# Kernel optimization log

Measured on AMD Instinct MI355X. Metric: run time of the kernel, lower is better.

The kernel has to match this reference:

```python
import jax, jax.numpy as jnp
import numpy as np

# FP8 E4M3 spike bits [S, E3..E0, M2 M1 M0] -> exact FP32 bits [S, E7..E0, M22..M0].
# FP8 bias 7, FP32 bias 127 => normal biased-FP32 exponent = e_fp8 + 120.
# Subnormal FP8 (e==0, m>0) is normalized: leading one at mantissa bit 2/1/0 maps to
# biased exponents 120/119/118 (the circuit's e_sub constants). The 4x4 mantissa
# product (<=225) always fits exactly in the 24-bit FP32 significand, so no rounding.

def _decode(X):
    # X: [..., 8] 0/1 floats. Returns sign, 4-bit significand (8..15, leading 1 at bit3),
    # biased FP32 exponent, and nonzero flag. All float32 except the bool flag.
    s = X[..., 0]
    e = X[..., 1] * 8.0 + X[..., 2] * 4.0 + X[..., 3] * 2.0 + X[..., 4]
    m = X[..., 5] * 4.0 + X[..., 6] * 2.0 + X[..., 7]
    normal = e > 0.0
    lead2 = m >= 4.0
    lead1 = (m >= 2.0) & (m < 4.0)
    frac_sub = jnp.where(lead2, m * 2.0, jnp.where(lead1, m * 4.0, m * 8.0))
    exp_sub = jnp.where(lead2, 120.0, jnp.where(lead1, 119.0, 118.0))
    frac = jnp.where(normal, m + 8.0, frac_sub)
    exp = jnp.where(normal, e + 120.0, exp_sub)
    nonzero = normal | (m > 0.0)
    return s, frac, exp, nonzero


def _fp8_mul_to_fp32_bits(A, B):
    A, B = jnp.broadcast_arrays(A, B)
    sa, fa, ea, nza = _decode(A)
    sb, fb, eb, nzb = _decode(B)
    s_out = jnp.mod(sa + sb, 2.0)                       # XOR of sign bits
    p = fa * fb                                         # 8-bit product in [64, 225]
    e_sum = ea + eb - 127.0
    carry = p >= 128.0                                  # leading one at bit 7 vs bit 6
    exp_out = jnp.where(carry, e_sum + 1.0, e_sum)
    # align fractional bits into the 23-bit FP32 mantissa (7 or 6 fraction bits)
    mant_out = jnp.where(carry, (p - 128.0) * 65536.0, (p - 64.0) * 131072.0)
    nz = nza & nzb
    exp_out = jnp.where(nz, exp_out, 0.0)               # true zero -> exp=0, mant=0
    mant_out = jnp.where(nz, mant_out, 0.0)
    exp_pow = 2.0 ** jnp.arange(7, -1, -1, dtype=jnp.float32)
    mant_pow = 2.0 ** jnp.arange(22, -1, -1, dtype=jnp.float32)
    exp_bits = jnp.mod(jnp.floor(exp_out[..., None] / exp_pow), 2.0)
    mant_bits = jnp.mod(jnp.floor(mant_out[..., None] / mant_pow), 2.0)
    return jnp.concatenate([s_out[..., None], exp_bits, mant_bits], axis=-1)


def setup_inputs() -> dict:
    key = jax.random.key(0)
    kA, kB = jax.random.split(key)
    A = jax.random.randint(kA, (1024, 4096, 8), 0, 2).astype(jnp.float32)
    B = jax.random.randint(kB, (1024, 4096, 8), 0, 2).astype(jnp.float32)
    return {"A": A, "B": B}


def reference(A, B):
    return _fp8_mul_to_fp32_bits(A, B)
```

## Files before the change

kernel.cpp:

```cpp
#include <hip/hip_runtime.h>
#include <stdint.h>


__device__ __forceinline__ uint32_t bit_of(float f) {
    return (__float_as_uint(f) >> 23) & 1u;
}

__device__ __forceinline__ void decode8(const float4 v0, const float4 v1,
                                        uint32_t& s, int& frac, int& exp, int& nz) {
    s = bit_of(v0.x);
    int e = (int)((bit_of(v0.y) << 3) | (bit_of(v0.z) << 2) |
                  (bit_of(v0.w) << 1) |  bit_of(v1.x));
    int m = (int)((bit_of(v1.y) << 2) | (bit_of(v1.z) << 1) | bit_of(v1.w));
    int frac_sub = (m >= 4) ? (m << 1) : ((m >= 2) ? (m << 2) : (m << 3));
    int exp_sub  = (m >= 4) ? 120      : ((m >= 2) ? 119      : 118);
    bool normal = (e > 0);
    frac = normal ? (m | 8)    : frac_sub;
    exp  = normal ? (e + 120)  : exp_sub;
    nz   = ((e | m) != 0) ? 1 : 0;
}

__global__ __launch_bounds__(256) void spike_fp8_mul_kernel(
        const float4* __restrict__ A, const float4* __restrict__ B,
        float4* __restrict__ out, int n_out4) {
    int j = blockIdx.x * blockDim.x + threadIdx.x;
    if (j >= n_out4) return;
    int elem = j >> 3;
    int g    = j & 7;

    float4 a0 = A[2 * elem], a1 = A[2 * elem + 1];
    float4 b0 = B[2 * elem], b1 = B[2 * elem + 1];

    uint32_t sa, sb; int fa, ea, fb, eb, nza, nzb;
    decode8(a0, a1, sa, fa, ea, nza);
    decode8(b0, b1, sb, fb, eb, nzb);

    uint32_t sign = sa ^ sb;
    int p = fa * fb;
    int carry = p >> 7;
    int exp_out = ea + eb - 127 + carry;
    uint32_t mant = ((uint32_t)p << (17 - carry)) & 0x7fffffu;
    uint32_t bits = (sign << 31) | ((uint32_t)exp_out << 23) | mant;
    if (!(nza & nzb)) bits = sign << 31;

    int sh = 31 - (g << 2);
    float4 o;
    o.x = ((bits >> sh)       & 1u) ? 1.0f : 0.0f;
    o.y = ((bits >> (sh - 1)) & 1u) ? 1.0f : 0.0f;
    o.z = ((bits >> (sh - 2)) & 1u) ? 1.0f : 0.0f;
    o.w = ((bits >> (sh - 3)) & 1u) ? 1.0f : 0.0f;
    out[j] = o;
}

extern "C" void kernel_launch(void* const* d_in, const int* in_sizes, int n_in,
                              void* d_out, int out_size, void* d_ws, size_t ws_size,
                              hipStream_t stream) {
    const float4* A = (const float4*)d_in[0];
    const float4* B = (const float4*)d_in[1];
    float4* out     = (float4*)d_out;
    int n_out4 = out_size / 4;
    const int block = 256;
    int grid = (n_out4 + block - 1) / block;
    hipLaunchKernelGGL(spike_fp8_mul_kernel, dim3(grid), dim3(block), 0, stream,
                       A, B, out, n_out4);
}
```

Measured before the change: 694.8 us.

## Compute one element per thread and redistribute output bits via wave shuffles

Each thread now loads and decodes a single FP8 pair once instead of eight threads redundantly loading and decoding the same element. The 32 output bits are spread across the wavefront with __shfl so each store instruction writes contiguous float4s across lanes, keeping writes coalesced. This removes the 8x redundant input loads and decode arithmetic, at the cost of 8 cross-lane shuffles per thread and an 8-iteration store loop with tail masking.

Result: faster. 672.8 us (-3.2%).

```diff
diff --git a/kernel.cpp b/kernel.cpp
--- a/kernel.cpp
+++ b/kernel.cpp
@@ -15,21 +15,20 @@
     int frac_sub = (m >= 4) ? (m << 1) : ((m >= 2) ? (m << 2) : (m << 3));
     int exp_sub  = (m >= 4) ? 120      : ((m >= 2) ? 119      : 118);
     bool normal = (e > 0);
-    frac = normal ? (m | 8)    : frac_sub;
-    exp  = normal ? (e + 120)  : exp_sub;
+    frac = normal ? (m | 8)   : frac_sub;
+    exp  = normal ? (e + 120) : exp_sub;
     nz   = ((e | m) != 0) ? 1 : 0;
 }
 
 __global__ __launch_bounds__(256) void spike_fp8_mul_kernel(
         const float4* __restrict__ A, const float4* __restrict__ B,
-        float4* __restrict__ out, int n_out4) {
-    int j = blockIdx.x * blockDim.x + threadIdx.x;
-    if (j >= n_out4) return;
-    int elem = j >> 3;
-    int g    = j & 7;
+        float4* __restrict__ out, int n_elem) {
+    int gid  = blockIdx.x * blockDim.x + threadIdx.x;
+    int lane = threadIdx.x & 63;
+    int lgid = (gid < n_elem) ? gid : (n_elem - 1);
 
-    float4 a0 = A[2 * elem], a1 = A[2 * elem + 1];
-    float4 b0 = B[2 * elem], b1 = B[2 * elem + 1];
+    float4 a0 = A[2 * lgid], a1 = A[2 * lgid + 1];
+    float4 b0 = B[2 * lgid], b1 = B[2 * lgid + 1];
 
     uint32_t sa, sb; int fa, ea, fb, eb, nza, nzb;
     decode8(a0, a1, sa, fa, ea, nza);
@@ -43,13 +42,25 @@
     uint32_t bits = (sign << 31) | ((uint32_t)exp_out << 23) | mant;
     if (!(nza & nzb)) bits = sign << 31;
 
-    int sh = 31 - (g << 2);
-    float4 o;
-    o.x = ((bits >> sh)       & 1u) ? 1.0f : 0.0f;
-    o.y = ((bits >> (sh - 1)) & 1u) ? 1.0f : 0.0f;
-    o.z = ((bits >> (sh - 2)) & 1u) ? 1.0f : 0.0f;
-    o.w = ((bits >> (sh - 3)) & 1u) ? 1.0f : 0.0f;
-    out[j] = o;
+    int we = gid - lane;
+    float4* wout = out + (size_t)we * 8;
+    int g   = lane & 7;
+    int src = lane >> 3;
+    uint32_t m0 = 1u << (31 - (g << 2));
+    uint32_t m1 = m0 >> 1, m2 = m0 >> 2, m3 = m0 >> 3;
+    long long lim = (long long)n_elem * 8;
+
+    #pragma unroll
+    for (int i = 0; i < 8; ++i) {
+        uint32_t ub = (uint32_t)__shfl((int)bits, i * 8 + src, 64);
+        float4 o;
+        o.x = (ub & m0) ? 1.0f : 0.0f;
+        o.y = (ub & m1) ? 1.0f : 0.0f;
+        o.z = (ub & m2) ? 1.0f : 0.0f;
+        o.w = (ub & m3) ? 1.0f : 0.0f;
+        long long j = (long long)we * 8 + i * 64 + lane;
+        if (j < lim) wout[i * 64 + lane] = o;
+    }
 }
 
 extern "C" void kernel_launch(void* const* d_in, const int* in_sizes, int n_in,
@@ -58,9 +69,9 @@
     const float4* A = (const float4*)d_in[0];
     const float4* B = (const float4*)d_in[1];
     float4* out     = (float4*)d_out;
-    int n_out4 = out_size / 4;
+    int n_elem = in_sizes[0] / 8;
     const int block = 256;
-    int grid = (n_out4 + block - 1) / block;
+    int grid = (n_elem + block - 1) / block;
     hipLaunchKernelGGL(spike_fp8_mul_kernel, dim3(grid), dim3(block), 0, stream,
-                       A, B, out, n_out4);
+                       A, B, out, n_elem);
 }
```
